# Kernel tuning notes

Hardware: AMD Instinct MI355X
Metric: run time of the kernel (lower is better)

Reference implementation:

```python
import jax, jax.numpy as jnp
import numpy as np

V = 32            # number_variables
K = 16            # degree + 1 spline coefficients per pair
DEG = 3           # cubic B-spline order for basis evaluation
LO, HI = -5.0, 5.0
SPAN_FACTOR = 0.1
N_SAMPLES = 131072
P_PAIRS = V * (V - 1) // 2  # 496


def bspline_basis(x):
    """Cubic B-spline basis with K clamped-uniform basis functions on the
    span_factor-expanded range [LO - s, HI + s].  x: [N] -> [N, K]."""
    s = SPAN_FACTOR * (HI - LO)
    lo, hi = LO - s, HI + s
    n_break = K - DEG + 1
    inner = jnp.linspace(lo, hi, n_break)
    t = jnp.concatenate([jnp.full((DEG,), lo), inner, jnp.full((DEG,), hi)])  # [K+DEG+1]
    x = jnp.clip(x, lo, hi - 1e-6 * (hi - lo))
    xb = x[:, None]
    # order-0 indicator functions: [N, K+DEG]
    B = ((xb >= t[None, :-1]) & (xb < t[None, 1:])).astype(x.dtype)
    for r in range(1, DEG + 1):
        tl, tr = t[:-(r + 1)], t[r:-1]
        den1 = tr - tl
        left = jnp.where(den1 > 0, (xb - tl) / jnp.where(den1 > 0, den1, 1.0), 0.0)
        tl2, tr2 = t[1:-r], t[r + 1:]
        den2 = tr2 - tl2
        right = jnp.where(den2 > 0, (tr2 - xb) / jnp.where(den2 > 0, den2, 1.0), 0.0)
        B = left * B[:, :-1] + right * B[:, 1:]
    return B  # [N, K]


def setup_inputs() -> dict:
    key = jax.random.key(0)
    k1, k2 = jax.random.split(key)
    inp = jax.random.normal(k1, (N_SAMPLES, V), dtype=jnp.float32)
    # learned spline coefficients, one column per (var, covar) pair,
    # initialized near the module's 0.1 constant init
    params = 0.1 + 0.05 * jax.random.normal(k2, (K, P_PAIRS), dtype=jnp.float32)
    return {"input": inp, "params": params}


def reference(input, params):
    # output[:, v] = input[:, v] + sum_{c < v} lambda_{v,c}(input[:, c]) * input[:, c]
    # In forward (non-inverse) mode every lambda depends only on `input`, so all
    # V*(V-1)/2 pairs are computed in one batched contraction instead of a loop.
    Basis = jax.vmap(bspline_basis)(input.T)  # [V, N, K], basis per covariate column
    idx_v, idx_c = np.tril_indices(V, -1)      # pair order matches params_index = v*(v-1)/2 + c
    P_mat = jnp.zeros((V, K, V), dtype=input.dtype).at[idx_c, :, idx_v].set(params.T)
    contrib = jnp.einsum('cnk,ckv->cnv', Basis, P_mat)   # lambda_{v,c}(x_{n,c})
    out = input + jnp.einsum('cnv,nc->nv', contrib, input)
    return out
```

## Files before the change

### kernel.cpp

```cpp
#include <hip/hip_runtime.h>
#include <hip/hip_bf16.h>


#define NSAMP 131072
#define PPAIR 496

typedef _Float16 f16x8 __attribute__((ext_vector_type(8)));
typedef float f32x4 __attribute__((ext_vector_type(4)));
typedef unsigned int uint32;
typedef unsigned short ushort16;

__global__ __launch_bounds__(256) void prep_w2t(const float* __restrict__ params,
                                                ushort16* __restrict__ w2t) {
    int idx = blockIdx.x * 256 + threadIdx.x;
    int v = idx >> 9;
    int ck = idx & 511;
    int c = ck >> 4, k = ck & 15;
    float w = 0.0f;
    if (c < v) w = params[k * PPAIR + (v * (v - 1)) / 2 + c];
    _Float16 h = (_Float16)w;
    w2t[idx] = __builtin_bit_cast(ushort16, h);
}

__device__ __forceinline__ float invden(int d) {
    return d == 1 ? (13.0f / 12.0f) : (d == 2 ? (13.0f / 24.0f) : (13.0f / 36.0f));
}

__global__ __launch_bounds__(256, 2) void decor_main(const float* __restrict__ xin,
                                                     const ushort16* __restrict__ w2t,
                                                     float* __restrict__ out) {
    __shared__ __align__(16) ushort16 G[4][16][520];

    const int tid = threadIdx.x;
    const int w = tid >> 6;
    const int l = tid & 63;
    const int s = l & 15;
    const int q = l >> 4;

    f16x8 bfrag[16][2];
#pragma unroll
    for (int t = 0; t < 16; ++t) {
#pragma unroll
        for (int nt = 0; nt < 2; ++nt) {
            int n = nt * 16 + s;
            bfrag[t][nt] = *(const f16x8*)(w2t + n * 512 + t * 32 + q * 8);
        }
    }

    const float lo = -6.0f;
    const float hk = 12.0f / 13.0f;
    const float inv_h = 13.0f / 12.0f;
    const float xmax = 6.0f - 1.2e-5f;

    uint32* const Gdw = (uint32*)&G[w][0][0];

    for (int tile = 0; tile < 4; ++tile) {
        const int S0 = blockIdx.x * 256 + w * 64 + tile * 16;

#pragma unroll
        for (int it = 0; it < 16; ++it) {
            int chunk = it * 64 + l;
            int row = chunk >> 6, ci = chunk & 63;
            *(uint4*)(Gdw + row * 260 + ci * 4) = make_uint4(0u, 0u, 0u, 0u);
        }

#pragma unroll
        for (int a = 0; a < 8; ++a) {
            int c = q + 4 * a;
            float x = xin[(S0 + s) * 32 + c];
            float xc = fminf(fmaxf(x, lo), xmax);
            float u = (xc - lo) * inv_h;
            int m = (int)u;
            m = m < 12 ? m : 12;

            int q0 = m - 2 > 0 ? m - 2 : 0;
            int q1 = m - 1 > 0 ? m - 1 : 0;
            int q4 = m + 2 < 13 ? m + 2 : 13;
            int q5 = m + 3 < 13 ? m + 3 : 13;
            float km  = fmaf((float)m,       hk, lo);
            float km1 = fmaf((float)(m + 1), hk, lo);
            float kq0 = fmaf((float)q0, hk, lo);
            float kq1 = fmaf((float)q1, hk, lo);
            float kq4 = fmaf((float)q4, hk, lo);
            float kq5 = fmaf((float)q5, hk, lo);
            float left1 = xc - km,  right1 = km1 - xc;
            float left2 = xc - kq1, right2 = kq4 - xc;
            float left3 = xc - kq0, right3 = kq5 - xc;

            float T, sv;
            T = 13.0f / 12.0f;
            float N0 = right1 * T;
            float N1 = left1 * T;
            T = N0 * invden((m + 1) - q1);
            N0 = right1 * T;
            sv = left2 * T;
            T = N1 * invden(q4 - m);
            N1 = fmaf(right2, T, sv);
            sv = left1 * T;
            float N2 = sv;
            T = N0 * invden((m + 1) - q0);
            N0 = right1 * T;
            sv = left3 * T;
            T = N1 * invden(q4 - q1);
            N1 = fmaf(right2, T, sv);
            sv = left2 * T;
            T = N2 * invden(q5 - m);
            N2 = fmaf(right3, T, sv);
            sv = left1 * T;
            float N3 = sv;

            float g0 = x * N0, g1 = x * N1, g2 = x * N2, g3 = x * N3;
            int e = m & 1;
            float a0 = e ? 0.0f : g0, b0 = e ? g0 : g1;
            float a1 = e ? g1 : g2,   b1 = e ? g2 : g3;
            uint32 d0 = __builtin_bit_cast(uint32, __builtin_amdgcn_cvt_pkrtz(a0, b0));
            uint32 d1 = __builtin_bit_cast(uint32, __builtin_amdgcn_cvt_pkrtz(a1, b1));
            uint32* rowp = (uint32*)&G[w][s][0];
            int dwb = c * 8 + (m >> 1);
            rowp[dwb] = d0;
            rowp[dwb + 1] = d1;
            if (e) {
                uint32 d2 = __builtin_bit_cast(uint32, __builtin_amdgcn_cvt_pkrtz(g3, 0.0f));
                rowp[dwb + 2] = d2;
            }
        }
        __syncthreads();

        f32x4 acc0 = {0.0f, 0.0f, 0.0f, 0.0f};
        f32x4 acc1 = {0.0f, 0.0f, 0.0f, 0.0f};
#pragma unroll
        for (int t = 0; t < 16; ++t) {
            f16x8 af = *(const f16x8*)&G[w][s][t * 32 + q * 8];
            acc0 = __builtin_amdgcn_mfma_f32_16x16x32_f16(af, bfrag[t][0], acc0, 0, 0, 0);
            acc1 = __builtin_amdgcn_mfma_f32_16x16x32_f16(af, bfrag[t][1], acc1, 0, 0, 0);
        }

#pragma unroll
        for (int r = 0; r < 4; ++r) {
            int sample = S0 + q * 4 + r;
            int base = sample * 32;
            out[base + s]      = xin[base + s]      + acc0[r];
            out[base + 16 + s] = xin[base + 16 + s] + acc1[r];
        }
        __syncthreads();
    }
}

extern "C" void kernel_launch(void* const* d_in, const int* in_sizes, int n_in,
                              void* d_out, int out_size, void* d_ws, size_t ws_size,
                              hipStream_t stream) {
    const float* xin = (const float*)d_in[0];
    const float* params = (const float*)d_in[1];
    float* out = (float*)d_out;
    ushort16* w2t = (ushort16*)d_ws;

    prep_w2t<<<64, 256, 0, stream>>>(params, w2t);
    decor_main<<<512, 256, 0, stream>>>(xin, w2t, out);
}
```

Measured before the change: 90.59 us.

## Build MFMA A-fragments in registers via lane shuffles instead of LDS staging

Replaces the shared-memory scratch matrix (zero-fill, scattered writes, barriers, reads) with direct register construction of the sparse basis A-fragments. Each lane permutes its packed basis values and exchanges halves with its partner lane via shuffles, and the B-fragments are reordered to match. It also skips the MFMAs for output columns 0-15 on the upper covariate chunks, since the lower-triangular weights make them zero there. A fast path uses the closed-form uniform cubic B-spline when the whole wave is in the interior. The cost is more register pressure and select logic, and correctness now depends on the intricate lane and k-ordering permutation matching the weight layout.

```diff
diff --git a/kernel.cpp b/kernel.cpp
--- a/kernel.cpp
+++ b/kernel.cpp
@@ -2,147 +2,167 @@
 #include <hip/hip_bf16.h>
 
 
-#define NSAMP 131072
 #define PPAIR 496
 
 typedef _Float16 f16x8 __attribute__((ext_vector_type(8)));
 typedef float f32x4 __attribute__((ext_vector_type(4)));
-typedef unsigned int uint32;
-typedef unsigned short ushort16;
+typedef unsigned int u32;
+typedef unsigned int u32x4 __attribute__((ext_vector_type(4)));
 
 __global__ __launch_bounds__(256) void prep_w2t(const float* __restrict__ params,
-                                                ushort16* __restrict__ w2t) {
+                                                unsigned short* __restrict__ w2t) {
     int idx = blockIdx.x * 256 + threadIdx.x;
     int v = idx >> 9;
-    int ck = idx & 511;
-    int c = ck >> 4, k = ck & 15;
+    int c = (idx >> 4) & 31, k = idx & 15;
     float w = 0.0f;
     if (c < v) w = params[k * PPAIR + (v * (v - 1)) / 2 + c];
     _Float16 h = (_Float16)w;
-    w2t[idx] = __builtin_bit_cast(ushort16, h);
-}
-
-__device__ __forceinline__ float invden(int d) {
-    return d == 1 ? (13.0f / 12.0f) : (d == 2 ? (13.0f / 24.0f) : (13.0f / 36.0f));
+    w2t[idx] = __builtin_bit_cast(unsigned short, h);
 }
 
 __global__ __launch_bounds__(256, 2) void decor_main(const float* __restrict__ xin,
-                                                     const ushort16* __restrict__ w2t,
+                                                     const unsigned short* __restrict__ w2t,
                                                      float* __restrict__ out) {
-    __shared__ __align__(16) ushort16 G[4][16][520];
-
     const int tid = threadIdx.x;
-    const int w = tid >> 6;
+    const int wv = tid >> 6;
     const int l = tid & 63;
     const int s = l & 15;
     const int q = l >> 4;
+    const int qp = q & 1;
+    const int sigma = ((q & 1) << 1) | (q >> 1);
 
-    f16x8 bfrag[16][2];
+    f16x8 b1[8][2];
+    f16x8 b0[4][2];
 #pragma unroll
-    for (int t = 0; t < 16; ++t) {
+    for (int u = 0; u < 8; ++u) {
 #pragma unroll
-        for (int nt = 0; nt < 2; ++nt) {
-            int n = nt * 16 + s;
-            bfrag[t][nt] = *(const f16x8*)(w2t + n * 512 + t * 32 + q * 8);
+        for (int e = 0; e < 2; ++e) {
+            int t = 2 * u + (qp ? (1 - e) : e);
+            b1[u][e] = *(const f16x8*)(w2t + (16 + s) * 512 + t * 32 + q * 8);
+            if (u < 4) b0[u][e] = *(const f16x8*)(w2t + s * 512 + t * 32 + q * 8);
         }
     }
 
-    const float lo = -6.0f;
-    const float hk = 12.0f / 13.0f;
-    const float inv_h = 13.0f / 12.0f;
-    const float xmax = 6.0f - 1.2e-5f;
-
-    uint32* const Gdw = (uint32*)&G[w][0][0];
+    const float xmax = 5.999988f;
+    const float sc = 13.0f / 12.0f;
 
     for (int tile = 0; tile < 4; ++tile) {
-        const int S0 = blockIdx.x * 256 + w * 64 + tile * 16;
+        const int S0 = blockIdx.x * 256 + wv * 64 + tile * 16;
+        const float* xrow = xin + (S0 + s) * 32 + sigma;
+        float xv[8];
+#pragma unroll
+        for (int u = 0; u < 8; ++u) xv[u] = xrow[4 * u];
+
+        f32x4 acc0 = {0.f, 0.f, 0.f, 0.f};
+        f32x4 acc1 = {0.f, 0.f, 0.f, 0.f};
 
 #pragma unroll
-        for (int it = 0; it < 16; ++it) {
-            int chunk = it * 64 + l;
-            int row = chunk >> 6, ci = chunk & 63;
-            *(uint4*)(Gdw + row * 260 + ci * 4) = make_uint4(0u, 0u, 0u, 0u);
+        for (int u = 0; u < 8; ++u) {
+            float x = xv[u];
+            float xc = fminf(fmaxf(x, -6.0f), xmax);
+            float uu = fmaf(xc, sc, 6.5f);
+            int mi = (int)uu;
+            mi = mi < 12 ? mi : 12;
+            float mf = (float)mi;
+            float r = uu - mf;
+            float N0, N1, N2, N3;
+            if (__all(mi >= 3 && mi <= 9)) {
+                float omr = 1.0f - r;
+                float r2 = r * r, r3 = r2 * r;
+                float o2 = omr * omr;
+                N0 = o2 * omr * (1.0f / 6.0f);
+                N3 = r3 * (1.0f / 6.0f);
+                N1 = fmaf(0.5f, r3, (2.0f / 3.0f) - r2);
+                N2 = 1.0f - N0 - N1 - N3;
+            } else {
+                float t13 = 13.0f - mf;
+                float af = fminf(mf, 1.0f);
+                float bf = fminf(mf, 2.0f);
+                float cf = fminf(t13, 2.0f);
+                float df = fminf(t13, 3.0f);
+                float r1 = 1.0f - r;
+                float l2 = r + af, rr2 = cf - r;
+                float l3 = r + bf, rr3 = df - r;
+                float iv = (af == 0.0f) ? 1.0f : 0.5f;
+                float T = r1 * iv;
+                float M0 = r1 * T;
+                float sv = l2 * T;
+                float iv2 = (cf == 1.0f) ? 1.0f : 0.5f;
+                float T2 = r * iv2;
+                float M1 = fmaf(rr2, T2, sv);
+                float M2 = r * T2;
+                float iv3 = 0.5f;
+                iv3 = (bf == 0.0f) ? 1.0f : iv3;
+                iv3 = (bf == 2.0f) ? (1.0f / 3.0f) : iv3;
+                T = M0 * iv3;
+                N0 = r1 * T;
+                sv = l3 * T;
+                float g14 = af + cf;
+                float iv4 = (g14 == 2.0f) ? 0.5f : (1.0f / 3.0f);
+                T = M1 * iv4;
+                N1 = fmaf(rr2, T, sv);
+                sv = l2 * T;
+                float iv5 = 0.5f;
+                iv5 = (df == 1.0f) ? 1.0f : iv5;
+                iv5 = (df == 3.0f) ? (1.0f / 3.0f) : iv5;
+                T = M2 * iv5;
+                N2 = fmaf(rr3, T, sv);
+                N3 = r * T;
+            }
+            float g0 = x * N0, g1 = x * N1, g2 = x * N2, g3 = x * N3;
+            int e = mi & 1;
+            float aa = e ? 0.0f : g0, bb = e ? g0 : g1;
+            float cc = e ? g1 : g2, dd = e ? g2 : g3;
+            float ee = e ? g3 : 0.0f;
+            u32 p0 = __builtin_bit_cast(u32, __builtin_amdgcn_cvt_pkrtz(aa, bb));
+            u32 p1 = __builtin_bit_cast(u32, __builtin_amdgcn_cvt_pkrtz(cc, dd));
+            u32 p2 = __builtin_bit_cast(u32, __builtin_amdgcn_cvt_pkrtz(ee, 0.0f));
+            int w0 = mi >> 1;
+            int dlt = w0 & 1;
+            u32 C0 = dlt ? 0u : p0;
+            u32 C1 = dlt ? p0 : p1;
+            u32 C2 = dlt ? p1 : p2;
+            u32 C3 = dlt ? p2 : 0u;
+            int j0 = (w0 & 6) ^ (qp << 2);
+            bool b2 = (j0 & 2) != 0;
+            u32 t0 = b2 ? 0u : C0;
+            u32 t1 = b2 ? 0u : C1;
+            u32 t2 = b2 ? C0 : C2;
+            u32 t3 = b2 ? C1 : C3;
+            u32 t4 = b2 ? C2 : 0u;
+            u32 t5 = b2 ? C3 : 0u;
+            bool b4 = (j0 & 4) != 0;
+            u32 B0 = b4 ? t4 : t0;
+            u32 B1 = b4 ? t5 : t1;
+            u32 B2 = b4 ? 0u : t2;
+            u32 B3 = b4 ? 0u : t3;
+            u32 B4 = b4 ? t0 : t4;
+            u32 B5 = b4 ? t1 : t5;
+            u32 B6 = b4 ? t2 : 0u;
+            u32 B7 = b4 ? t3 : 0u;
+            u32 R0 = (u32)__shfl_xor((int)B4, 16);
+            u32 R1 = (u32)__shfl_xor((int)B5, 16);
+            u32 R2 = (u32)__shfl_xor((int)B6, 16);
+            u32 R3 = (u32)__shfl_xor((int)B7, 16);
+            u32x4 kp = {B0, B1, B2, B3};
+            u32x4 rc = {R0, R1, R2, R3};
+            f16x8 ka = __builtin_bit_cast(f16x8, kp);
+            f16x8 ra = __builtin_bit_cast(f16x8, rc);
+            acc1 = __builtin_amdgcn_mfma_f32_16x16x32_f16(ka, b1[u][0], acc1, 0, 0, 0);
+            acc1 = __builtin_amdgcn_mfma_f32_16x16x32_f16(ra, b1[u][1], acc1, 0, 0, 0);
+            if (u < 4) {
+                acc0 = __builtin_amdgcn_mfma_f32_16x16x32_f16(ka, b0[u][0], acc0, 0, 0, 0);
+                acc0 = __builtin_amdgcn_mfma_f32_16x16x32_f16(ra, b0[u][1], acc0, 0, 0, 0);
+            }
         }
 
 #pragma unroll
-        for (int a = 0; a < 8; ++a) {
-            int c = q + 4 * a;
-            float x = xin[(S0 + s) * 32 + c];
-            float xc = fminf(fmaxf(x, lo), xmax);
-            float u = (xc - lo) * inv_h;
-            int m = (int)u;
-            m = m < 12 ? m : 12;
-
-            int q0 = m - 2 > 0 ? m - 2 : 0;
-            int q1 = m - 1 > 0 ? m - 1 : 0;
-            int q4 = m + 2 < 13 ? m + 2 : 13;
-            int q5 = m + 3 < 13 ? m + 3 : 13;
-            float km  = fmaf((float)m,       hk, lo);
-            float km1 = fmaf((float)(m + 1), hk, lo);
-            float kq0 = fmaf((float)q0, hk, lo);
-            float kq1 = fmaf((float)q1, hk, lo);
-            float kq4 = fmaf((float)q4, hk, lo);
-            float kq5 = fmaf((float)q5, hk, lo);
-            float left1 = xc - km,  right1 = km1 - xc;
-            float left2 = xc - kq1, right2 = kq4 - xc;
-            float left3 = xc - kq0, right3 = kq5 - xc;
-
-            float T, sv;
-            T = 13.0f / 12.0f;
-            float N0 = right1 * T;
-            float N1 = left1 * T;
-            T = N0 * invden((m + 1) - q1);
-            N0 = right1 * T;
-            sv = left2 * T;
-            T = N1 * invden(q4 - m);
-            N1 = fmaf(right2, T, sv);
-            sv = left1 * T;
-            float N2 = sv;
-            T = N0 * invden((m + 1) - q0);
-            N0 = right1 * T;
-            sv = left3 * T;
-            T = N1 * invden(q4 - q1);
-            N1 = fmaf(right2, T, sv);
-            sv = left2 * T;
-            T = N2 * invden(q5 - m);
-            N2 = fmaf(right3, T, sv);
-            sv = left1 * T;
-            float N3 = sv;
-
-            float g0 = x * N0, g1 = x * N1, g2 = x * N2, g3 = x * N3;
-            int e = m & 1;
-            float a0 = e ? 0.0f : g0, b0 = e ? g0 : g1;
-            float a1 = e ? g1 : g2,   b1 = e ? g2 : g3;
-            uint32 d0 = __builtin_bit_cast(uint32, __builtin_amdgcn_cvt_pkrtz(a0, b0));
-            uint32 d1 = __builtin_bit_cast(uint32, __builtin_amdgcn_cvt_pkrtz(a1, b1));
-            uint32* rowp = (uint32*)&G[w][s][0];
-            int dwb = c * 8 + (m >> 1);
-            rowp[dwb] = d0;
-            rowp[dwb + 1] = d1;
-            if (e) {
-                uint32 d2 = __builtin_bit_cast(uint32, __builtin_amdgcn_cvt_pkrtz(g3, 0.0f));
-                rowp[dwb + 2] = d2;
-            }
+        for (int rI = 0; rI < 4; ++rI) {
+            int sample = S0 + q * 4 + rI;
+            int base = sample * 32;
+            out[base + s]      = xin[base + s]      + acc0[rI];
+            out[base + 16 + s] = xin[base + 16 + s] + acc1[rI];
         }
-        __syncthreads();
-
-        f32x4 acc0 = {0.0f, 0.0f, 0.0f, 0.0f};
-        f32x4 acc1 = {0.0f, 0.0f, 0.0f, 0.0f};
-#pragma unroll
-        for (int t = 0; t < 16; ++t) {
-            f16x8 af = *(const f16x8*)&G[w][s][t * 32 + q * 8];
-            acc0 = __builtin_amdgcn_mfma_f32_16x16x32_f16(af, bfrag[t][0], acc0, 0, 0, 0);
-            acc1 = __builtin_amdgcn_mfma_f32_16x16x32_f16(af, bfrag[t][1], acc1, 0, 0, 0);
-        }
-
-#pragma unroll
-        for (int r = 0; r < 4; ++r) {
-            int sample = S0 + q * 4 + r;
-            int base = sample * 32;
-            out[base + s]      = xin[base + s]      + acc0[r];
-            out[base + 16 + s] = xin[base + 16 + s] + acc1[r];
-        }
-        __syncthreads();
     }
 }
 
@@ -152,7 +172,7 @@
     const float* xin = (const float*)d_in[0];
     const float* params = (const float*)d_in[1];
     float* out = (float*)d_out;
-    ushort16* w2t = (ushort16*)d_ws;
+    unsigned short* w2t = (unsigned short*)d_ws;
 
     prep_w2t<<<64, 256, 0, stream>>>(params, w2t);
     decor_main<<<512, 256, 0, stream>>>(xin, w2t, out);
```

After: 85.32 us. 1.06x faster.
